# Optimization experiments

Measured on AMD Instinct MI355X. Metric: run time of the kernel, lower is better.

Reference implementation:

```python
import jax, jax.numpy as jnp
import numpy as np

N_GRAPHS = 100
NODES_PER_GRAPH = 1000
N = N_GRAPHS * NODES_PER_GRAPH
DEG = 16
E = N * DEG
IN_FEATS = 64
HIDDEN = 128
READOUT_DIM = HIDDEN // 2
SLOPE = 0.01
EPS = 1e-5


def leaky(x):
    return jnp.where(x >= 0, x, SLOPE * x)


def _kaiming(k, shape):
    # torch kaiming_uniform_, fan_in mode, leaky_relu gain
    fan_in = shape[0]
    gain = np.sqrt(2.0 / (1.0 + SLOPE ** 2))
    bound = gain * np.sqrt(3.0 / fan_in)
    return jax.random.uniform(k, shape, jnp.float32, -bound, bound)


def setup_inputs() -> dict:
    key = jax.random.key(0)
    ks = jax.random.split(key, 16)
    node_feats = jax.random.normal(ks[0], (N, IN_FEATS), jnp.float32)
    # within-graph random edges (batched graph of equal-sized components)
    src_local = jax.random.randint(ks[1], (E,), 0, NODES_PER_GRAPH)
    dst_local = jax.random.randint(ks[2], (E,), 0, NODES_PER_GRAPH)
    edge_graph = jnp.repeat(jnp.arange(N_GRAPHS, dtype=jnp.int32), E // N_GRAPHS)
    src = (edge_graph * NODES_PER_GRAPH + src_local).astype(jnp.int32)
    dst = (edge_graph * NODES_PER_GRAPH + dst_local).astype(jnp.int32)
    edge_weights = jax.random.uniform(ks[3], (E,), jnp.float32)
    node_graph = jnp.repeat(jnp.arange(N_GRAPHS, dtype=jnp.int32), NODES_PER_GRAPH)
    return {
        "node_feats": node_feats,
        "edge_weights": edge_weights,
        "W1": _kaiming(ks[4], (IN_FEATS, HIDDEN)),
        "W2": _kaiming(ks[5], (HIDDEN, HIDDEN)),
        "gn1_alpha": jnp.ones((HIDDEN,), jnp.float32),
        "gn1_gamma": jnp.ones((HIDDEN,), jnp.float32),
        "gn1_beta": jnp.zeros((HIDDEN,), jnp.float32),
        "gn2_alpha": jnp.ones((HIDDEN,), jnp.float32),
        "gn2_gamma": jnp.ones((HIDDEN,), jnp.float32),
        "gn2_beta": jnp.zeros((HIDDEN,), jnp.float32),
        "r1_w1": _kaiming(ks[6], (HIDDEN, HIDDEN)),
        "r1_b1": jnp.zeros((HIDDEN,), jnp.float32),
        "r1_w2": _kaiming(ks[7], (HIDDEN, READOUT_DIM)),
        "r1_b2": jnp.zeros((READOUT_DIM,), jnp.float32),
        "r2_w1": _kaiming(ks[8], (HIDDEN, HIDDEN)),
        "r2_b1": jnp.zeros((HIDDEN,), jnp.float32),
        "r2_w2": _kaiming(ks[9], (HIDDEN, READOUT_DIM)),
        "r2_b2": jnp.zeros((READOUT_DIM,), jnp.float32),
        "src": src,
        "dst": dst,
        "node_graph": node_graph,
    }


def _graph_conv(x, W, src, dst, ew, out_isqrt, in_isqrt):
    # DGL GraphConv norm='both', no bias: D_in^{-1/2} A_w D_out^{-1/2} X W
    h = (x * out_isqrt[:, None]) @ W                 # [N, out]
    m = h[src] * ew[:, None]                         # [E, out] gather + edge weight
    agg = jax.ops.segment_sum(m, dst, num_segments=N)  # scatter-add
    return agg * in_isqrt[:, None]


def _graph_norm(x, alpha, gamma, beta, node_graph, inv_cnt):
    mean = jax.ops.segment_sum(x, node_graph, num_segments=N_GRAPHS) * inv_cnt
    sub = x - alpha * mean[node_graph]
    var = jax.ops.segment_sum(sub * sub, node_graph, num_segments=N_GRAPHS) * inv_cnt
    return gamma * sub / jnp.sqrt(var[node_graph] + EPS) + beta


def _readout(x, w1, b1, w2, b2, node_graph, inv_cnt):
    # deep-sets style universal readout: rho(mean(phi(h_v)))
    h = leaky(x @ w1 + b1)
    pooled = jax.ops.segment_sum(h, node_graph, num_segments=N_GRAPHS) * inv_cnt
    return leaky(pooled @ w2 + b2)


def reference(node_feats, edge_weights, W1, W2,
              gn1_alpha, gn1_gamma, gn1_beta,
              gn2_alpha, gn2_gamma, gn2_beta,
              r1_w1, r1_b1, r1_w2, r1_b2,
              r2_w1, r2_b1, r2_w2, r2_b2,
              src, dst, node_graph):
    ones_e = jnp.ones((E,), jnp.float32)
    out_deg = jnp.clip(jax.ops.segment_sum(ones_e, src, num_segments=N), 1.0)
    in_deg = jnp.clip(jax.ops.segment_sum(ones_e, dst, num_segments=N), 1.0)
    out_isqrt = jax.lax.rsqrt(out_deg)
    in_isqrt = jax.lax.rsqrt(in_deg)
    inv_cnt = 1.0 / NODES_PER_GRAPH

    h = _graph_conv(node_feats, W1, src, dst, edge_weights, out_isqrt, in_isqrt)
    h = leaky(_graph_norm(h, gn1_alpha, gn1_gamma, gn1_beta, node_graph, inv_cnt))
    # dropout is identity in eval mode
    r1 = _readout(h, r1_w1, r1_b1, r1_w2, r1_b2, node_graph, inv_cnt)
    m1 = jax.ops.segment_sum(h, node_graph, num_segments=N_GRAPHS) * inv_cnt

    h = _graph_conv(h, W2, src, dst, edge_weights, out_isqrt, in_isqrt)
    h = leaky(_graph_norm(h, gn2_alpha, gn2_gamma, gn2_beta, node_graph, inv_cnt))
    r2 = _readout(h, r2_w1, r2_b1, r2_w2, r2_b2, node_graph, inv_cnt)
    m2 = jax.ops.segment_sum(h, node_graph, num_segments=N_GRAPHS) * inv_cnt

    readout = jnp.concatenate([r1, m1, r2, m2], axis=1)  # [G, 2*H + 2*H/2] = [100, 384]
    return leaky(readout)
```

## Files before the change

kernel.cpp:

```cpp
#include <hip/hip_runtime.h>
#include <cstddef>
#include <cstdint>

#define NG   100
#define NPG  1000
#define NN   (NG * NPG)
#define NE   (NN * 16)
#define EPG  (NE / NG)
#define CSRG 20000
#define FIN  64
#define HID  128
#define RD   64
#define SLOPE 0.01f
#define EPSV  1e-5f
#define NSTRIP 250
#define GSN   40

using short8 = __attribute__((ext_vector_type(8))) short;
using f32x4  = __attribute__((ext_vector_type(4))) float;
typedef unsigned short u16;

__device__ __forceinline__ float leaky(float x) { return x >= 0.f ? x : SLOPE * x; }

__device__ __forceinline__ u16 f2bf(float f) {
  union { float f; unsigned u; } v; v.f = f;
  return (u16)((v.u + 0x7fffu + ((v.u >> 16) & 1u)) >> 16);
}
__device__ __forceinline__ float bf2f(u16 u) {
  union { unsigned u; float f; } v; v.u = ((unsigned)u) << 16;
  return v.f;
}

__device__ __forceinline__ bool swz(int b, int per_g, int& g, int& part) {
  const int xcd = b & 7;
  const int slot = b >> 3;
  g = xcd + 8 * (slot / per_g);
  part = slot % per_g;
  return g < NG;
}

__global__ __launch_bounds__(256) void wt_k(const float* __restrict__ W1,
                                            const float* __restrict__ W2,
                                            const float* __restrict__ R1,
                                            const float* __restrict__ R2,
                                            u16* __restrict__ Wt1,
                                            u16* __restrict__ Wt2,
                                            u16* __restrict__ Rt1,
                                            u16* __restrict__ Rt2) {
  const int idx = blockIdx.x * 256 + threadIdx.x;
  if (idx < FIN * HID) {
    const int n = idx >> 6, k = idx & 63;
    Wt1[idx] = f2bf(W1[k * HID + n]);
  } else {
    const int j = idx - FIN * HID;
    const int m = j >> 14, r = j & 16383;
    const int n = r >> 7, k = r & 127;
    const float* s = (m == 0) ? W2 : (m == 1) ? R1 : R2;
    u16* d = (m == 0) ? Wt2 : (m == 1) ? Rt1 : Rt2;
    d[r] = f2bf(s[k * HID + n]);
  }
}

__global__ __launch_bounds__(1024) void build_k(const int* __restrict__ src,
                                                const int* __restrict__ dst,
                                                const float* __restrict__ ew,
                                                int* __restrict__ cin_,
                                                int* __restrict__ cout_,
                                                int* __restrict__ offs,
                                                unsigned* __restrict__ csr) {
  __shared__ int hin[NPG];
  __shared__ int hout[NPG];
  __shared__ int cur[NPG];
  __shared__ int wtot[16];
  int g, part;
  if (!swz(blockIdx.x, 1, g, part)) return;
  const int t = threadIdx.x;
  const int lane = t & 63, wave = t >> 6;
  const int nb = g * NPG, eb = g * EPG;
  if (t < NPG) { hin[t] = 0; hout[t] = 0; }
  __syncthreads();
  for (int e = t; e < EPG; e += 4096) {
    int s4[4], d4[4];
#pragma unroll
    for (int k = 0; k < 4; ++k) {
      const int ee = e + k * 1024;
      if (ee < EPG) { s4[k] = src[eb + ee]; d4[k] = dst[eb + ee]; }
      else d4[k] = -1;
    }
#pragma unroll
    for (int k = 0; k < 4; ++k)
      if (d4[k] >= 0) {
        atomicAdd(&hout[s4[k] - nb], 1);
        atomicAdd(&hin[d4[k] - nb], 1);
      }
  }
  __syncthreads();
  int v[4], vr[4];
  int loc = 0;
#pragma unroll
  for (int k = 0; k < 4; ++k) {
    const int idx = t * 4 + k;
    v[k] = (idx < NPG) ? hin[idx] : 0;
    vr[k] = (v[k] + 3) & ~3;
    loc += vr[k];
  }
  int incl = loc;
#pragma unroll
  for (int d = 1; d < 64; d <<= 1) {
    const int x = __shfl_up(incl, d);
    if (lane >= d) incl += x;
  }
  if (lane == 63) wtot[wave] = incl;
  if (t < NPG) { cin_[nb + t] = hin[t]; cout_[nb + t] = hout[t]; }
  __syncthreads();
  int wexc = 0;
  for (int i = 0; i < wave; ++i) wexc += wtot[i];
  int run = g * CSRG + wexc + (incl - loc);
#pragma unroll
  for (int k = 0; k < 4; ++k) {
    const int idx = t * 4 + k;
    if (idx < NPG) {
      offs[nb + idx] = run;
      cur[idx] = run;
      run += vr[k];
    }
  }
  __syncthreads();
  for (int e = t; e < EPG; e += 4096) {
    int s4[4], d4[4]; float w4[4];
#pragma unroll
    for (int k = 0; k < 4; ++k) {
      const int ee = e + k * 1024;
      if (ee < EPG) { s4[k] = src[eb + ee]; d4[k] = dst[eb + ee]; w4[k] = ew[eb + ee]; }
      else d4[k] = -1;
    }
#pragma unroll
    for (int k = 0; k < 4; ++k)
      if (d4[k] >= 0) {
        const int pos = atomicAdd(&cur[d4[k] - nb], 1);
        csr[pos] = ((unsigned)(s4[k] - nb) << 16) | (unsigned)f2bf(w4[k]);
      }
  }
}

__global__ __launch_bounds__(256) void gemm1_k(const float* __restrict__ X,
                                               const u16* __restrict__ Wt,
                                               const int* __restrict__ cout_,
                                               u16* __restrict__ Y) {
  __shared__ u16 Xl[64 * FIN];
  __shared__ u16 Wl[HID * FIN];
  const int tid = threadIdx.x;
  const int wave = tid >> 6, lane = tid & 63, l15 = lane & 15, quad = lane >> 4;
  int g, part;
  if (!swz(blockIdx.x, 4, g, part)) return;
  const int base = g * NPG + part * NSTRIP;
  const int kq = tid & 15;
  const int srow = tid >> 4;

  for (int i = tid; i < HID * (FIN / 8); i += 256) {
    const int n = i >> 3, c = i & 7;
    const short8 w = *(const short8*)(Wt + n * FIN + c * 8);
    *(short8*)&Wl[n * FIN + ((c ^ (n & 7)) << 3)] = w;
  }
  float4 xpre[4];
#pragma unroll
  for (int it = 0; it < 4; ++it) {
    const int rowi = srow + it * 16;
    xpre[it] = (rowi < NSTRIP) ? *(const float4*)(X + (size_t)(base + rowi) * FIN + kq * 4)
                               : make_float4(0.f, 0.f, 0.f, 0.f);
  }
  for (int pass = 0; pass < 4; ++pass) {
    __syncthreads();
#pragma unroll
    for (int it = 0; it < 4; ++it) {
      const int r = srow + it * 16;
      ushort4 u = make_ushort4(f2bf(xpre[it].x), f2bf(xpre[it].y),
                               f2bf(xpre[it].z), f2bf(xpre[it].w));
      const int c = kq >> 1, half = kq & 1;
      *(ushort4*)&Xl[r * FIN + (((c ^ (r & 7)) << 3) | (half << 2))] = u;
    }
    __syncthreads();
    if (pass < 3) {
#pragma unroll
      for (int it = 0; it < 4; ++it) {
        const int rowi = (pass + 1) * 64 + srow + it * 16;
        xpre[it] = (rowi < NSTRIP) ? *(const float4*)(X + (size_t)(base + rowi) * FIN + kq * 4)
                                   : make_float4(0.f, 0.f, 0.f, 0.f);
      }
    }
    short8 a[2];
    const int arow = wave * 16 + l15;
#pragma unroll
    for (int kt = 0; kt < 2; ++kt)
      a[kt] = *(const short8*)&Xl[arow * FIN + (((kt * 4 + quad) ^ (l15 & 7)) << 3)];
    float sc[4];
    int rows[4];
#pragma unroll
    for (int r = 0; r < 4; ++r) {
      rows[r] = pass * 64 + wave * 16 + quad * 4 + r;
      sc[r] = (rows[r] < NSTRIP) ? rsqrtf(fmaxf((float)cout_[base + rows[r]], 1.0f)) : 0.f;
    }
#pragma unroll
    for (int ct = 0; ct < 8; ++ct) {
      f32x4 acc = {0.f, 0.f, 0.f, 0.f};
      const int brow = ct * 16 + l15;
#pragma unroll
      for (int kt = 0; kt < 2; ++kt) {
        const short8 b = *(const short8*)&Wl[brow * FIN + (((kt * 4 + quad) ^ (l15 & 7)) << 3)];
        acc = __builtin_amdgcn_mfma_f32_16x16x32_bf16(a[kt], b, acc, 0, 0, 0);
      }
      const int n = ct * 16 + l15;
#pragma unroll
      for (int r = 0; r < 4; ++r)
        if (rows[r] < NSTRIP) Y[(size_t)(base + rows[r]) * HID + n] = f2bf(acc[r] * sc[r]);
    }
  }
}

__device__ __forceinline__ void norm_affine(const float* sx, const float* sq,
                                            const float* alpha, const float* gamma,
                                            const float* beta, int g, int c8,
                                            float* Av, float* Bv) {
  const float inv = 1.0f / NPG;
#pragma unroll
  for (int j = 0; j < 8; ++j) {
    const int f = c8 * 8 + j;
    const float mean = sx[g * HID + f] * inv;
    const float ex2 = sq[g * HID + f] * inv;
    const float am = alpha[f] * mean;
    const float var = fmaxf(ex2 - 2.0f * am * mean + am * am, 0.0f);
    const float A = gamma[f] * rsqrtf(var + EPSV);
    Av[j] = A;
    Bv[j] = beta[f] - A * am;
  }
}

__global__ __launch_bounds__(256) void gemm_norm_k(const u16* __restrict__ Xb,
                                                   const u16* __restrict__ Wt,
                                                   const float* __restrict__ sx,
                                                   const float* __restrict__ sq,
                                                   const float* __restrict__ alpha,
                                                   const float* __restrict__ gamma,
                                                   const float* __restrict__ beta,
                                                   const int* __restrict__ cout_,
                                                   u16* __restrict__ Y) {
  __shared__ u16 Xl[64 * HID];
  __shared__ u16 Wl[HID * HID];
  const int tid = threadIdx.x;
  const int wave = tid >> 6, lane = tid & 63, l15 = lane & 15, quad = lane >> 4;
  int g, part;
  if (!swz(blockIdx.x, 4, g, part)) return;
  const int base = g * NPG + part * NSTRIP;
  const int c8 = tid & 15;
  const int srow = tid >> 4;

  for (int i = tid; i < HID * (HID / 8); i += 256) {
    const int n = i >> 4, c = i & 15;
    const short8 w = *(const short8*)(Wt + n * HID + c * 8);
    *(short8*)&Wl[n * HID + ((c ^ (n & 15)) << 3)] = w;
  }
  float Av[8], Bv[8];
  norm_affine(sx, sq, alpha, gamma, beta, g, c8, Av, Bv);
  const short8 z8 = {0, 0, 0, 0, 0, 0, 0, 0};
  short8 xpre[4];
#pragma unroll
  for (int it = 0; it < 4; ++it) {
    const int rowi = srow + it * 16;
    xpre[it] = (rowi < NSTRIP) ? *(const short8*)(Xb + (size_t)(base + rowi) * HID + c8 * 8) : z8;
  }
  for (int pass = 0; pass < 4; ++pass) {
    __syncthreads();
#pragma unroll
    for (int it = 0; it < 4; ++it) {
      const int r = srow + it * 16;
      const int rowi = pass * 64 + r;
      short8 o = z8;
      if (rowi < NSTRIP) {
#pragma unroll
        for (int j = 0; j < 8; ++j)
          o[j] = (short)f2bf(leaky(fmaf(Av[j], bf2f((u16)xpre[it][j]), Bv[j])));
      }
      *(short8*)&Xl[r * HID + ((c8 ^ (r & 15)) << 3)] = o;
    }
    __syncthreads();
    if (pass < 3) {
#pragma unroll
      for (int it = 0; it < 4; ++it) {
        const int rowi = (pass + 1) * 64 + srow + it * 16;
        xpre[it] = (rowi < NSTRIP) ? *(const short8*)(Xb + (size_t)(base + rowi) * HID + c8 * 8) : z8;
      }
    }
    short8 a[4];
    const int arow = wave * 16 + l15;
#pragma unroll
    for (int kt = 0; kt < 4; ++kt)
      a[kt] = *(const short8*)&Xl[arow * HID + (((kt * 4 + quad) ^ l15) << 3)];
    float sc[4];
    int rows[4];
#pragma unroll
    for (int r = 0; r < 4; ++r) {
      rows[r] = pass * 64 + wave * 16 + quad * 4 + r;
      sc[r] = (rows[r] < NSTRIP) ? rsqrtf(fmaxf((float)cout_[base + rows[r]], 1.0f)) : 0.f;
    }
#pragma unroll
    for (int ct = 0; ct < 8; ++ct) {
      f32x4 acc = {0.f, 0.f, 0.f, 0.f};
      const int brow = ct * 16 + l15;
#pragma unroll
      for (int kt = 0; kt < 4; ++kt) {
        const short8 b = *(const short8*)&Wl[brow * HID + (((kt * 4 + quad) ^ l15) << 3)];
        acc = __builtin_amdgcn_mfma_f32_16x16x32_bf16(a[kt], b, acc, 0, 0, 0);
      }
      const int n = ct * 16 + l15;
#pragma unroll
      for (int r = 0; r < 4; ++r)
        if (rows[r] < NSTRIP) Y[(size_t)(base + rows[r]) * HID + n] = f2bf(acc[r] * sc[r]);
    }
  }
}

struct RedT { float red[16][HID]; float hred[16][HID]; };
union ShT { u16 Xl[64 * HID]; RedT r; };

__global__ __launch_bounds__(256) void phi_pool_k(const u16* __restrict__ Xb,
                                                  const float* __restrict__ sx,
                                                  const float* __restrict__ sq,
                                                  const float* __restrict__ alpha,
                                                  const float* __restrict__ gamma,
                                                  const float* __restrict__ beta,
                                                  const u16* __restrict__ Wt,
                                                  const float* __restrict__ b1,
                                                  float* __restrict__ phi_sum,
                                                  float* __restrict__ h_sum) {
  __shared__ ShT sh;
  __shared__ u16 Wl[HID * HID];
  const int tid = threadIdx.x;
  const int wave = tid >> 6, lane = tid & 63, l15 = lane & 15, quad = lane >> 4;
  int g, part;
  if (!swz(blockIdx.x, 4, g, part)) return;
  const int base = g * NPG + part * NSTRIP;
  const int c8 = tid & 15;
  const int srow = tid >> 4;

  for (int i = tid; i < HID * (HID / 8); i += 256) {
    const int n = i >> 4, c = i & 15;
    const short8 w = *(const short8*)(Wt + n * HID + c * 8);
    *(short8*)&Wl[n * HID + ((c ^ (n & 15)) << 3)] = w;
  }
  float Av[8], Bv[8];
  norm_affine(sx, sq, alpha, gamma, beta, g, c8, Av, Bv);
  float bcol[8];
#pragma unroll
  for (int ct = 0; ct < 8; ++ct) bcol[ct] = b1[ct * 16 + l15];

  float pooled[8] = {0.f, 0.f, 0.f, 0.f, 0.f, 0.f, 0.f, 0.f};
  float hp[8] = {0.f, 0.f, 0.f, 0.f, 0.f, 0.f, 0.f, 0.f};
  const short8 z8 = {0, 0, 0, 0, 0, 0, 0, 0};
  short8 xpre[4];
#pragma unroll
  for (int it = 0; it < 4; ++it) {
    const int rowi = srow + it * 16;
    xpre[it] = (rowi < NSTRIP) ? *(const short8*)(Xb + (size_t)(base + rowi) * HID + c8 * 8) : z8;
  }
  for (int pass = 0; pass < 4; ++pass) {
    __syncthreads();
#pragma unroll
    for (int it = 0; it < 4; ++it) {
      const int r = srow + it * 16;
      const int rowi = pass * 64 + r;
      short8 o = z8;
      if (rowi < NSTRIP) {
#pragma unroll
        for (int j = 0; j < 8; ++j) {
          const float xn = leaky(fmaf(Av[j], bf2f((u16)xpre[it][j]), Bv[j]));
          hp[j] += xn;
          o[j] = (short)f2bf(xn);
        }
      }
      *(short8*)&sh.Xl[r * HID + ((c8 ^ (r & 15)) << 3)] = o;
    }
    __syncthreads();
    if (pass < 3) {
#pragma unroll
      for (int it = 0; it < 4; ++it) {
        const int rowi = (pass + 1) * 64 + srow + it * 16;
        xpre[it] = (rowi < NSTRIP) ? *(const short8*)(Xb + (size_t)(base + rowi) * HID + c8 * 8) : z8;
      }
    }
    short8 a[4];
    const int arow = wave * 16 + l15;
#pragma unroll
    for (int kt = 0; kt < 4; ++kt)
      a[kt] = *(const short8*)&sh.Xl[arow * HID + (((kt * 4 + quad) ^ l15) << 3)];
#pragma unroll
    for (int ct = 0; ct < 8; ++ct) {
      f32x4 acc = {0.f, 0.f, 0.f, 0.f};
      const int brow = ct * 16 + l15;
#pragma unroll
      for (int kt = 0; kt < 4; ++kt) {
        const short8 b = *(const short8*)&Wl[brow * HID + (((kt * 4 + quad) ^ l15) << 3)];
        acc = __builtin_amdgcn_mfma_f32_16x16x32_bf16(a[kt], b, acc, 0, 0, 0);
      }
#pragma unroll
      for (int r = 0; r < 4; ++r) {
        const int rowi = pass * 64 + wave * 16 + quad * 4 + r;
        if (rowi < NSTRIP) pooled[ct] += leaky(acc[r] + bcol[ct]);
      }
    }
  }
  __syncthreads();
  const int qi = wave * 4 + quad;
#pragma unroll
  for (int ct = 0; ct < 8; ++ct) sh.r.red[qi][ct * 16 + l15] = pooled[ct];
#pragma unroll
  for (int j = 0; j < 8; ++j) sh.r.hred[tid >> 4][(tid & 15) * 8 + j] = hp[j];
  __syncthreads();
  if (tid < HID) {
    float s = 0.f;
#pragma unroll
    for (int q = 0; q < 16; ++q) s += sh.r.red[q][tid];
    unsafeAtomicAdd(&phi_sum[g * HID + tid], s);
  } else {
    const int t = tid - HID;
    float s = 0.f;
#pragma unroll
    for (int rr = 0; rr < 16; ++rr) s += sh.r.hred[rr][t];
    unsafeAtomicAdd(&h_sum[g * HID + t], s);
  }
}

__global__ __launch_bounds__(256) void gather_k(const u16* __restrict__ H,
                                                const unsigned* __restrict__ csr,
                                                const int* __restrict__ offs,
                                                const int* __restrict__ cin_,
                                                u16* __restrict__ AGG,
                                                float* __restrict__ sx,
                                                float* __restrict__ sq) {
  __shared__ float redx[4][HID];
  __shared__ float redq[4][HID];
  const int wave = threadIdx.x >> 6;
  const int lane = threadIdx.x & 63;
  int g, part;
  if (!swz(blockIdx.x, 25, g, part)) return;
  const int nb = g * NPG;
  const int base = nb + part * GSN;
  const int loff = lane * 2;
  const u16* __restrict__ Hg = H + (size_t)nb * HID;

  float sxa = 0.f, sxb = 0.f, sqa = 0.f, sqb = 0.f;
  for (int it = 0; it < 3; ++it) {
    const int nc = (it < 2) ? 4 : 2;
    int nn[4], off[4], cnt[4], c4[4];
    float isq[4];
    const uint4* p[4];
#pragma unroll
    for (int c = 0; c < 4; ++c) {
      const int j = it * 4 + c;
      const int node = base + wave + ((j < 10) ? j : 0) * 4;
      nn[c] = node;
      const int nu = __builtin_amdgcn_readfirstlane(node);
      off[c] = __builtin_amdgcn_readfirstlane(offs[nu]);
      cnt[c] = (c < nc) ? __builtin_amdgcn_readfirstlane(cin_[nu]) : 0;
      c4[c] = cnt[c] >> 2;
      isq[c] = rsqrtf(fmaxf((float)cnt[c], 1.0f));
      p[c] = (const uint4*)__builtin_assume_aligned(csr + off[c], 16);
    }
    float ax[4] = {0.f, 0.f, 0.f, 0.f};
    float ay[4] = {0.f, 0.f, 0.f, 0.f};
    int common = min(c4[0], c4[1]);
    if (nc == 4) common = min(common, min(c4[2], c4[3]));
    for (int t = 0; t < common; ++t) {
      uint4 r[4];
      unsigned u[4][4];
#pragma unroll
      for (int c = 0; c < 4; ++c)
        if (c < nc) {
          r[c] = p[c][t];
          u[c][0] = *(const unsigned*)(Hg + (size_t)(r[c].x >> 16) * HID + loff);
          u[c][1] = *(const unsigned*)(Hg + (size_t)(r[c].y >> 16) * HID + loff);
          u[c][2] = *(const unsigned*)(Hg + (size_t)(r[c].z >> 16) * HID + loff);
          u[c][3] = *(const unsigned*)(Hg + (size_t)(r[c].w >> 16) * HID + loff);
        }
#pragma unroll
      for (int c = 0; c < 4; ++c)
        if (c < nc) {
          const float w0 = bf2f((u16)(r[c].x & 0xffffu));
          const float w1 = bf2f((u16)(r[c].y & 0xffffu));
          const float w2 = bf2f((u16)(r[c].z & 0xffffu));
          const float w3 = bf2f((u16)(r[c].w & 0xffffu));
          ax[c] = fmaf(w0, __uint_as_float(u[c][0] << 16), ax[c]);
          ay[c] = fmaf(w0, __uint_as_float(u[c][0] & 0xffff0000u), ay[c]);
          ax[c] = fmaf(w1, __uint_as_float(u[c][1] << 16), ax[c]);
          ay[c] = fmaf(w1, __uint_as_float(u[c][1] & 0xffff0000u), ay[c]);
          ax[c] = fmaf(w2, __uint_as_float(u[c][2] << 16), ax[c]);
          ay[c] = fmaf(w2, __uint_as_float(u[c][2] & 0xffff0000u), ay[c]);
          ax[c] = fmaf(w3, __uint_as_float(u[c][3] << 16), ax[c]);
          ay[c] = fmaf(w3, __uint_as_float(u[c][3] & 0xffff0000u), ay[c]);
        }
    }
#pragma unroll
    for (int c = 0; c < 4; ++c) {
      for (int t = common; t < c4[c]; ++t) {
        const uint4 r = p[c][t];
        const unsigned u0 = *(const unsigned*)(Hg + (size_t)(r.x >> 16) * HID + loff);
        const unsigned u1 = *(const unsigned*)(Hg + (size_t)(r.y >> 16) * HID + loff);
        const unsigned u2 = *(const unsigned*)(Hg + (size_t)(r.z >> 16) * HID + loff);
        const unsigned u3 = *(const unsigned*)(Hg + (size_t)(r.w >> 16) * HID + loff);
        const float w0 = bf2f((u16)(r.x & 0xffffu));
        const float w1 = bf2f((u16)(r.y & 0xffffu));
        const float w2 = bf2f((u16)(r.z & 0xffffu));
        const float w3 = bf2f((u16)(r.w & 0xffffu));
        ax[c] = fmaf(w0, __uint_as_float(u0 << 16), ax[c]);
        ay[c] = fmaf(w0, __uint_as_float(u0 & 0xffff0000u), ay[c]);
        ax[c] = fmaf(w1, __uint_as_float(u1 << 16), ax[c]);
        ay[c] = fmaf(w1, __uint_as_float(u1 & 0xffff0000u), ay[c]);
        ax[c] = fmaf(w2, __uint_as_float(u2 << 16), ax[c]);
        ay[c] = fmaf(w2, __uint_as_float(u2 & 0xffff0000u), ay[c]);
        ax[c] = fmaf(w3, __uint_as_float(u3 << 16), ax[c]);
        ay[c] = fmaf(w3, __uint_as_float(u3 & 0xffff0000u), ay[c]);
      }
      for (int k = c4[c] << 2; k < cnt[c]; ++k) {
        const unsigned r0 = csr[off[c] + k];
        const float w = bf2f((u16)(r0 & 0xffffu));
        const unsigned u0 = *(const unsigned*)(Hg + (size_t)(r0 >> 16) * HID + loff);
        ax[c] = fmaf(w, __uint_as_float(u0 << 16), ax[c]);
        ay[c] = fmaf(w, __uint_as_float(u0 & 0xffff0000u), ay[c]);
      }
    }
#pragma unroll
    for (int c = 0; c < 4; ++c)
      if (c < nc) {
        const float rx = ax[c] * isq[c];
        const float ry = ay[c] * isq[c];
        *(unsigned*)(AGG + (size_t)nn[c] * HID + loff) =
            (unsigned)f2bf(rx) | ((unsigned)f2bf(ry) << 16);
        sxa += rx; sxb += ry;
        sqa += rx * rx; sqb += ry * ry;
      }
  }
  redx[wave][loff] = sxa; redx[wave][loff + 1] = sxb;
  redq[wave][loff] = sqa; redq[wave][loff + 1] = sqb;
  __syncthreads();
  const int tid = threadIdx.x;
  if (tid < HID) {
    unsafeAtomicAdd(&sx[g * HID + tid],
                    redx[0][tid] + redx[1][tid] + redx[2][tid] + redx[3][tid]);
  } else {
    const int t = tid - HID;
    unsafeAtomicAdd(&sq[g * HID + t],
                    redq[0][t] + redq[1][t] + redq[2][t] + redq[3][t]);
  }
}

__global__ __launch_bounds__(64) void finalize_k(const float* __restrict__ phi_sum,
                                                 const float* __restrict__ h_sum,
                                                 const float* __restrict__ w2,
                                                 const float* __restrict__ b2,
                                                 float* __restrict__ out,
                                                 int roff, int moff) {
  const int g = blockIdx.x;
  const int j = threadIdx.x;
  float acc = b2[j];
#pragma unroll 8
  for (int k = 0; k < HID; ++k)
    acc += (phi_sum[g * HID + k] * (1.0f / NPG)) * w2[k * RD + j];
  const float r = leaky(acc);
  out[g * 384 + roff + j] = leaky(r);
  out[g * 384 + moff + j] = leaky(h_sum[g * HID + j] * (1.0f / NPG));
  out[g * 384 + moff + 64 + j] = leaky(h_sum[g * HID + 64 + j] * (1.0f / NPG));
}

extern "C" void kernel_launch(void* const* d_in, const int* in_sizes, int n_in,
                              void* d_out, int out_size, void* d_ws, size_t ws_size,
                              hipStream_t stream) {
  const float* node_feats = (const float*)d_in[0];
  const float* ew   = (const float*)d_in[1];
  const float* W1   = (const float*)d_in[2];
  const float* W2   = (const float*)d_in[3];
  const float* g1a  = (const float*)d_in[4];
  const float* g1g  = (const float*)d_in[5];
  const float* g1b  = (const float*)d_in[6];
  const float* g2a  = (const float*)d_in[7];
  const float* g2g  = (const float*)d_in[8];
  const float* g2b  = (const float*)d_in[9];
  const float* r1w1 = (const float*)d_in[10];
  const float* r1b1 = (const float*)d_in[11];
  const float* r1w2 = (const float*)d_in[12];
  const float* r1b2 = (const float*)d_in[13];
  const float* r2w1 = (const float*)d_in[14];
  const float* r2b1 = (const float*)d_in[15];
  const float* r2w2 = (const float*)d_in[16];
  const float* r2b2 = (const float*)d_in[17];
  const int* src = (const int*)d_in[18];
  const int* dst = (const int*)d_in[19];
  float* out = (float*)d_out;

  char* wsb = (char*)d_ws;
  float* ps1     = (float*)wsb;
  float* hs1     = ps1 + NG * HID;
  float* ps2     = hs1 + NG * HID;
  float* hs2     = ps2 + NG * HID;
  float* sx1     = hs2 + NG * HID;
  float* sq1     = sx1 + NG * HID;
  float* sx2     = sq1 + NG * HID;
  float* sq2     = sx2 + NG * HID;
  int*   cin     = (int*)(sq2 + NG * HID);
  int*   cout_   = cin + NN;
  int*   offs    = cout_ + NN;
  unsigned* csr  = (unsigned*)(offs + NN);
  u16*   Wt1     = (u16*)(csr + (size_t)NG * CSRG);
  u16*   Wt2     = Wt1 + HID * FIN;
  u16*   Rt1     = Wt2 + HID * HID;
  u16*   Rt2     = Rt1 + HID * HID;
  u16*   bufA    = Rt2 + HID * HID;
  u16*   bufB    = bufA + (size_t)NN * HID;

  hipMemsetAsync(d_ws, 0, (size_t)(8 * NG * HID) * sizeof(float), stream);

  wt_k<<<(FIN * HID + 3 * HID * HID) / 256, 256, 0, stream>>>(
      W1, W2, r1w1, r2w1, Wt1, Wt2, Rt1, Rt2);
  build_k<<<8 * 13, 1024, 0, stream>>>(src, dst, ew, cin, cout_, offs, csr);

  const int gemm_grid = 8 * 4 * 13;
  const int gather_grid = 8 * 25 * 13;

  gemm1_k<<<gemm_grid, 256, 0, stream>>>(node_feats, Wt1, cout_, bufA);
  gather_k<<<gather_grid, 256, 0, stream>>>(bufA, csr, offs, cin, bufB, sx1, sq1);
  phi_pool_k<<<gemm_grid, 256, 0, stream>>>(bufB, sx1, sq1, g1a, g1g, g1b,
                                            Rt1, r1b1, ps1, hs1);
  finalize_k<<<NG, 64, 0, stream>>>(ps1, hs1, r1w2, r1b2, out, 0, 64);

  gemm_norm_k<<<gemm_grid, 256, 0, stream>>>(bufB, Wt2, sx1, sq1, g1a, g1g, g1b,
                                             cout_, bufA);
  gather_k<<<gather_grid, 256, 0, stream>>>(bufA, csr, offs, cin, bufB, sx2, sq2);
  phi_pool_k<<<gemm_grid, 256, 0, stream>>>(bufB, sx2, sq2, g2a, g2g, g2b,
                                            Rt2, r2b1, ps2, hs2);
  finalize_k<<<NG, 64, 0, stream>>>(ps2, hs2, r2w2, r2b2, out, 192, 256);
}
```

Before: 295.0 us.

## Split CSR build into parallel hist/scan/fill kernels and pad rows to fixed minimum

Replaces the single per-graph build kernel, which ran one 1024-thread block per graph, with three kernels: a global-atomic histogram over all edges, a per-graph scan, and an edge-parallel fill using global cursors. This spreads CSR construction across many more blocks. It also pads each CSR row to at least 20 entries with zero records, so the gather loop can run a fixed unrolled 5-iteration common part and drop its scalar tail loop. In exchange it adds global atomics, two extra launches, a larger memset, and wasted gathers on the padded zero entries, which read node 0 with weight zero.

```diff
diff --git a/kernel.cpp b/kernel.cpp
--- a/kernel.cpp
+++ b/kernel.cpp
@@ -7,7 +7,8 @@
 #define NN   (NG * NPG)
 #define NE   (NN * 16)
 #define EPG  (NE / NG)
-#define CSRG 20000
+#define CSRG 40000
+#define MINREC 20
 #define FIN  64
 #define HID  128
 #define RD   64
@@ -61,47 +62,35 @@
   }
 }
 
-__global__ __launch_bounds__(1024) void build_k(const int* __restrict__ src,
-                                                const int* __restrict__ dst,
-                                                const float* __restrict__ ew,
-                                                int* __restrict__ cin_,
-                                                int* __restrict__ cout_,
-                                                int* __restrict__ offs,
-                                                unsigned* __restrict__ csr) {
-  __shared__ int hin[NPG];
-  __shared__ int hout[NPG];
-  __shared__ int cur[NPG];
-  __shared__ int wtot[16];
+__global__ __launch_bounds__(256) void hist_k(const int* __restrict__ src,
+                                              const int* __restrict__ dst,
+                                              int* __restrict__ cout_,
+                                              int* __restrict__ cin_) {
+  const int e = blockIdx.x * 256 + threadIdx.x;
+  if (e < NE) {
+    atomicAdd(&cout_[src[e]], 1);
+    atomicAdd(&cin_[dst[e]], 1);
+  }
+}
+
+__global__ __launch_bounds__(256) void scan2_k(const int* __restrict__ cin_,
+                                               int* __restrict__ offs,
+                                               int* __restrict__ cursor,
+                                               unsigned* __restrict__ csr) {
+  __shared__ int wtot[4];
   int g, part;
   if (!swz(blockIdx.x, 1, g, part)) return;
   const int t = threadIdx.x;
   const int lane = t & 63, wave = t >> 6;
-  const int nb = g * NPG, eb = g * EPG;
-  if (t < NPG) { hin[t] = 0; hout[t] = 0; }
-  __syncthreads();
-  for (int e = t; e < EPG; e += 4096) {
-    int s4[4], d4[4];
-#pragma unroll
-    for (int k = 0; k < 4; ++k) {
-      const int ee = e + k * 1024;
-      if (ee < EPG) { s4[k] = src[eb + ee]; d4[k] = dst[eb + ee]; }
-      else d4[k] = -1;
-    }
-#pragma unroll
-    for (int k = 0; k < 4; ++k)
-      if (d4[k] >= 0) {
-        atomicAdd(&hout[s4[k] - nb], 1);
-        atomicAdd(&hin[d4[k] - nb], 1);
-      }
-  }
-  __syncthreads();
+  const int nb = g * NPG;
   int v[4], vr[4];
   int loc = 0;
 #pragma unroll
   for (int k = 0; k < 4; ++k) {
     const int idx = t * 4 + k;
-    v[k] = (idx < NPG) ? hin[idx] : 0;
-    vr[k] = (v[k] + 3) & ~3;
+    v[k] = (idx < NPG) ? cin_[nb + idx] : 0;
+    const int c4 = (v[k] + 3) & ~3;
+    vr[k] = (idx < NPG) ? ((c4 > MINREC) ? c4 : MINREC) : 0;
     loc += vr[k];
   }
   int incl = loc;
@@ -111,7 +100,6 @@
     if (lane >= d) incl += x;
   }
   if (lane == 63) wtot[wave] = incl;
-  if (t < NPG) { cin_[nb + t] = hin[t]; cout_[nb + t] = hout[t]; }
   __syncthreads();
   int wexc = 0;
   for (int i = 0; i < wave; ++i) wexc += wtot[i];
@@ -121,26 +109,29 @@
     const int idx = t * 4 + k;
     if (idx < NPG) {
       offs[nb + idx] = run;
-      cur[idx] = run;
+      cursor[nb + idx] = run;
+      for (int z = v[k]; z < vr[k]; ++z) csr[run + z] = 0;
       run += vr[k];
     }
   }
-  __syncthreads();
-  for (int e = t; e < EPG; e += 4096) {
-    int s4[4], d4[4]; float w4[4];
-#pragma unroll
-    for (int k = 0; k < 4; ++k) {
-      const int ee = e + k * 1024;
-      if (ee < EPG) { s4[k] = src[eb + ee]; d4[k] = dst[eb + ee]; w4[k] = ew[eb + ee]; }
-      else d4[k] = -1;
-    }
-#pragma unroll
-    for (int k = 0; k < 4; ++k)
-      if (d4[k] >= 0) {
-        const int pos = atomicAdd(&cur[d4[k] - nb], 1);
-        csr[pos] = ((unsigned)(s4[k] - nb) << 16) | (unsigned)f2bf(w4[k]);
-      }
-  }
+}
+
+__global__ __launch_bounds__(256) void fill_k(const int* __restrict__ src,
+                                              const int* __restrict__ dst,
+                                              const float* __restrict__ ew,
+                                              int* __restrict__ cursor,
+                                              unsigned* __restrict__ csr) {
+  int g, part;
+  if (!swz(blockIdx.x, 63, g, part)) return;
+  const int e0 = part * 256 + threadIdx.x;
+  if (e0 >= EPG) return;
+  const int nb = g * NPG;
+  const int e = g * EPG + e0;
+  const int s = src[e];
+  const int d = dst[e];
+  const float w = ew[e];
+  const int pos = atomicAdd(&cursor[d], 1);
+  csr[pos] = ((unsigned)(s - nb) << 16) | (unsigned)f2bf(w);
 }
 
 __global__ __launch_bounds__(256) void gemm1_k(const float* __restrict__ X,
@@ -450,7 +441,7 @@
   float sxa = 0.f, sxb = 0.f, sqa = 0.f, sqb = 0.f;
   for (int it = 0; it < 3; ++it) {
     const int nc = (it < 2) ? 4 : 2;
-    int nn[4], off[4], cnt[4], c4[4];
+    int nn[4], off[4], cnt[4], c4p[4];
     float isq[4];
     const uint4* p[4];
 #pragma unroll
@@ -461,15 +452,15 @@
       const int nu = __builtin_amdgcn_readfirstlane(node);
       off[c] = __builtin_amdgcn_readfirstlane(offs[nu]);
       cnt[c] = (c < nc) ? __builtin_amdgcn_readfirstlane(cin_[nu]) : 0;
-      c4[c] = cnt[c] >> 2;
+      const int cr = (cnt[c] + 3) & ~3;
+      c4p[c] = ((cr > MINREC) ? cr : MINREC) >> 2;
       isq[c] = rsqrtf(fmaxf((float)cnt[c], 1.0f));
       p[c] = (const uint4*)__builtin_assume_aligned(csr + off[c], 16);
     }
     float ax[4] = {0.f, 0.f, 0.f, 0.f};
     float ay[4] = {0.f, 0.f, 0.f, 0.f};
-    int common = min(c4[0], c4[1]);
-    if (nc == 4) common = min(common, min(c4[2], c4[3]));
-    for (int t = 0; t < common; ++t) {
+#pragma unroll
+    for (int t = 0; t < 5; ++t) {
       uint4 r[4];
       unsigned u[4][4];
 #pragma unroll
@@ -500,7 +491,7 @@
     }
 #pragma unroll
     for (int c = 0; c < 4; ++c) {
-      for (int t = common; t < c4[c]; ++t) {
+      for (int t = 5; t < c4p[c]; ++t) {
         const uint4 r = p[c][t];
         const unsigned u0 = *(const unsigned*)(Hg + (size_t)(r.x >> 16) * HID + loff);
         const unsigned u1 = *(const unsigned*)(Hg + (size_t)(r.y >> 16) * HID + loff);
@@ -518,13 +509,6 @@
         ay[c] = fmaf(w2, __uint_as_float(u2 & 0xffff0000u), ay[c]);
         ax[c] = fmaf(w3, __uint_as_float(u3 << 16), ax[c]);
         ay[c] = fmaf(w3, __uint_as_float(u3 & 0xffff0000u), ay[c]);
-      }
-      for (int k = c4[c] << 2; k < cnt[c]; ++k) {
-        const unsigned r0 = csr[off[c] + k];
-        const float w = bf2f((u16)(r0 & 0xffffu));
-        const unsigned u0 = *(const unsigned*)(Hg + (size_t)(r0 >> 16) * HID + loff);
-        ax[c] = fmaf(w, __uint_as_float(u0 << 16), ax[c]);
-        ay[c] = fmaf(w, __uint_as_float(u0 & 0xffff0000u), ay[c]);
       }
     }
 #pragma unroll
@@ -607,7 +591,8 @@
   int*   cin     = (int*)(sq2 + NG * HID);
   int*   cout_   = cin + NN;
   int*   offs    = cout_ + NN;
-  unsigned* csr  = (unsigned*)(offs + NN);
+  int*   cursor  = offs + NN;
+  unsigned* csr  = (unsigned*)(cursor + NN);
   u16*   Wt1     = (u16*)(csr + (size_t)NG * CSRG);
   u16*   Wt2     = Wt1 + HID * FIN;
   u16*   Rt1     = Wt2 + HID * HID;
@@ -615,11 +600,15 @@
   u16*   bufA    = Rt2 + HID * HID;
   u16*   bufB    = bufA + (size_t)NN * HID;
 
-  hipMemsetAsync(d_ws, 0, (size_t)(8 * NG * HID) * sizeof(float), stream);
+  const size_t zero_bytes = (size_t)(8 * NG * HID) * sizeof(float) +
+                            (size_t)(2 * NN) * sizeof(int);
+  hipMemsetAsync(d_ws, 0, zero_bytes, stream);
 
   wt_k<<<(FIN * HID + 3 * HID * HID) / 256, 256, 0, stream>>>(
       W1, W2, r1w1, r2w1, Wt1, Wt2, Rt1, Rt2);
-  build_k<<<8 * 13, 1024, 0, stream>>>(src, dst, ew, cin, cout_, offs, csr);
+  hist_k<<<(NE + 255) / 256, 256, 0, stream>>>(src, dst, cout_, cin);
+  scan2_k<<<8 * 13, 256, 0, stream>>>(cin, offs, cursor, csr);
+  fill_k<<<8 * 63 * 13, 256, 0, stream>>>(src, dst, ew, cursor, csr);
 
   const int gemm_grid = 8 * 4 * 13;
   const int gather_grid = 8 * 25 * 13;
```

New measurement: 426.3 us. +44.5%, slower.
